# Kernel tuning notes

Measured on AMD Instinct MI355X. Metric: run time of the kernel, lower is better.

The kernel has to match this reference:

```python
import jax, jax.numpy as jnp
import numpy as np

VARIANCE = (0.1, 0.2)   # SSD variance from init_kwargs
TOP_K = 1000            # max detections / NMS candidates per (image, class)


def _pairwise_iou(b):
    # b: [K,4] in point form (x1,y1,x2,y2)
    area = jnp.maximum(b[:, 2] - b[:, 0], 0.0) * jnp.maximum(b[:, 3] - b[:, 1], 0.0)
    lt = jnp.maximum(b[:, None, :2], b[None, :, :2])
    rb = jnp.minimum(b[:, None, 2:], b[None, :, 2:])
    wh = jnp.maximum(rb - lt, 0.0)
    inter = wh[..., 0] * wh[..., 1]
    union = area[:, None] + area[None, :] - inter
    return inter / jnp.maximum(union, 1e-12)


def _nms_pack(points, csboxes, scores, conf_thresh, nms_thresh):
    # points/csboxes: [P,4]; scores: [P]. Returns [TOP_K, 5] = (score, cx, cy, w, h)
    K = TOP_K
    masked = jnp.where(scores >= conf_thresh, scores, -jnp.inf)
    vals, idx = jax.lax.top_k(masked, K)          # sorted descending
    p = points[idx]                                # [K,4] point form
    cs = csboxes[idx]                              # [K,4] center-size form
    valid = vals >= conf_thresh
    iou = _pairwise_iou(p)                         # [K,K]
    ar = jnp.arange(K)

    def body(i, keep):
        # box i (if kept) suppresses all lower-scored boxes with IoU > thresh
        sup = (iou[i] > nms_thresh) & (ar > i) & keep[i]
        return keep & ~sup

    keep = jax.lax.fori_loop(0, K, body, valid)
    rows = jnp.concatenate([vals[:, None], cs], axis=1)        # [K,5]
    pos = jnp.where(keep, jnp.cumsum(keep) - 1, K)             # compact kept rows to front
    out = jnp.zeros((K, 5), rows.dtype).at[pos].set(rows, mode='drop')
    return out


def setup_inputs() -> dict:
    key = jax.random.key(0)
    k1, k2, k3, k4 = jax.random.split(key, 4)
    B, P, C = 8, 120000, 5
    loc_data = jax.random.normal(k1, (B, 4, P), dtype=jnp.float32) * 0.5
    conf_data = jax.random.normal(k2, (B, C, P), dtype=jnp.float32)
    cxcy = jax.random.uniform(k3, (P, 2), dtype=jnp.float32)
    wh = 0.01 + 0.29 * jax.random.uniform(k4, (P, 2), dtype=jnp.float32)
    prior_data = jnp.concatenate([cxcy, wh], axis=1)           # (cx,cy,w,h) in [0,1]
    return {
        'loc_data': loc_data,
        'conf_data': conf_data,
        'prior_data': prior_data,
        'conf_thresh': jnp.float32(0.05),
        'nms_thresh': jnp.float32(0.5),
    }


def reference(loc_data, conf_data, prior_data, conf_thresh, nms_thresh):
    v0, v1 = VARIANCE
    # softmax over class dim, drop background class 0 -> [B, Cfg, P]
    conf = jax.nn.softmax(conf_data, axis=1)[:, 1:]
    loc = jnp.transpose(loc_data, (0, 2, 1))                   # [B,P,4]
    # SSD decode -> center-size boxes
    cxcy = prior_data[None, :, :2] + loc[..., :2] * v0 * prior_data[None, :, 2:]
    wh = prior_data[None, :, 2:] * jnp.exp(loc[..., 2:] * v1)
    cs = jnp.concatenate([cxcy, wh], axis=-1)                  # [B,P,4] center-size
    pts = jnp.concatenate([cxcy - wh / 2, cxcy + wh / 2], axis=-1)  # [B,P,4] point form
    per_class = jax.vmap(_nms_pack, in_axes=(None, None, 0, None, None))
    per_image = jax.vmap(per_class, in_axes=(0, 0, 0, None, None))
    return per_image(pts, cs, conf, conf_thresh, nms_thresh)   # [B, Cfg, TOP_K, 5]
```

## Files before the change

### kernel.cpp

```cpp
#include <hip/hip_runtime.h>
#include <cstdint>
#include <cstddef>

typedef unsigned long long ull;

#define KTOP   1000
#define CAP    4096
#define HBITS  14
#define HB     (1 << HBITS)
#define HSHIFT (32 - HBITS)
#define ROWS   1024
#define WORDS  16
#define HCHUNK 16

__global__ void decode_kernel(const float* __restrict__ loc,
                              const float* __restrict__ conf,
                              const float* __restrict__ prior,
                              float* __restrict__ scores,
                              float* __restrict__ cs,
                              unsigned* __restrict__ histz,
                              int histW,
                              int B, int C, int P) {
#pragma clang fp contract(off)
    int t = blockIdx.x * blockDim.x + threadIdx.x;

    for (int i = t; i < histW; i += gridDim.x * blockDim.x) histz[i] = 0u;

    if (t >= B * P) return;
    int b = t / P;
    int p = t - b * P;

    float x[8];
    float m = -INFINITY;
    for (int c = 0; c < C; ++c) {
        x[c] = conf[((size_t)b * C + c) * P + p];
        m = fmaxf(m, x[c]);
    }
    float sum = 0.f;
    for (int c = 0; c < C; ++c) {
        x[c] = expf(x[c] - m);
        sum += x[c];
    }
    for (int c = 1; c < C; ++c) {
        float v = x[c] / sum;
        int bc = b * (C - 1) + (c - 1);
        scores[(size_t)bc * P + p] = v;
    }

    float l0 = loc[((size_t)b * 4 + 0) * P + p];
    float l1 = loc[((size_t)b * 4 + 1) * P + p];
    float l2 = loc[((size_t)b * 4 + 2) * P + p];
    float l3 = loc[((size_t)b * 4 + 3) * P + p];
    float4 pr4 = *(const float4*)(prior + (size_t)p * 4);

    float cx = pr4.x + (l0 * 0.1f) * pr4.z;
    float cy = pr4.y + (l1 * 0.1f) * pr4.w;
    float w  = pr4.z * expf(l2 * 0.2f);
    float h  = pr4.w * expf(l3 * 0.2f);

    *(float4*)(cs + ((size_t)b * P + p) * 4) = make_float4(cx, cy, w, h);
}

__global__ void __launch_bounds__(256)
hist_kernel(const float* __restrict__ scores,
            const float* __restrict__ cthp,
            unsigned* __restrict__ hist,
            int P) {
    __shared__ unsigned sh[HB / 2];
    int bc  = blockIdx.x;
    int tid = threadIdx.x;
    float cth = *cthp;

    for (int i = tid; i < HB / 2; i += 256) sh[i] = 0u;
    __syncthreads();

    int chunk = (P + HCHUNK - 1) / HCHUNK;
    int lo = blockIdx.y * chunk;
    int hi = lo + chunk; if (hi > P) hi = P;
    const float* s = scores + (size_t)bc * P;
    for (int p = lo + tid; p < hi; p += 256) {
        float v = s[p];
        if (v >= cth) {
            unsigned bin = __float_as_uint(v) >> HSHIFT;
            atomicAdd(&sh[bin >> 1], (bin & 1u) ? 65536u : 1u);
        }
    }
    __syncthreads();

    unsigned* h = hist + (size_t)bc * HB;
    for (int i = tid; i < HB / 2; i += 256) {
        unsigned v = sh[i];
        if (v & 0xFFFFu)  atomicAdd(&h[2 * i],     v & 0xFFFFu);
        if (v >> 16)      atomicAdd(&h[2 * i + 1], v >> 16);
    }
}

__global__ void __launch_bounds__(256)
pivot_kernel(const unsigned* __restrict__ hist, unsigned* __restrict__ pivot) {
    int bc  = blockIdx.x;
    int t   = threadIdx.x;
    const unsigned* h = hist + (size_t)bc * HB;
    __shared__ unsigned T[256];

    const int per = HB / 256;
    int base = t * per;
    unsigned S = 0;
    for (int i = 0; i < per; ++i) S += h[base + i];
    T[t] = S;
    __syncthreads();

    for (int d = 1; d < 256; d <<= 1) {
        unsigned add = (t + d < 256) ? T[t + d] : 0u;
        __syncthreads();
        T[t] += add;
        __syncthreads();
    }

    unsigned Tt = T[t];
    unsigned Tn = (t + 1 < 256) ? T[t + 1] : 0u;
    if (Tt >= (unsigned)KTOP && Tn < (unsigned)KTOP) {
        unsigned cum = Tn;
        for (int i = per - 1; i >= 0; --i) {
            cum += h[base + i];
            if (cum >= (unsigned)KTOP) { pivot[bc] = (unsigned)(base + i); break; }
        }
    }
    if (t == 0 && T[0] < (unsigned)KTOP) pivot[bc] = 0u;
}

__global__ void __launch_bounds__(256)
gather_kernel(const float* __restrict__ scores,
              const unsigned* __restrict__ pivot,
              unsigned* __restrict__ cnt,
              ull* __restrict__ cand,
              const float* __restrict__ cthp, int P) {
    __shared__ unsigned wsum[4];
    __shared__ unsigned s_base;
    int bc = blockIdx.x;
    const float* s = scores + (size_t)bc * P;
    float cth = *cthp;
    unsigned pv = pivot[bc];
    int nchunk = gridDim.y;
    int chunk = (P + nchunk - 1) / nchunk;
    int lo = blockIdx.y * chunk;
    int hi = lo + chunk; if (hi > P) hi = P;
    int tid  = threadIdx.x;
    int lane = tid & 63;
    int wid  = tid >> 6;

    unsigned mycnt = 0;
    for (int p = lo + tid; p < hi; p += 256) {
        float v = s[p];
        unsigned k = __float_as_uint(v);
        if (v >= cth && (k >> HSHIFT) >= pv) ++mycnt;
    }
    unsigned x = mycnt;
    for (int d = 1; d < 64; d <<= 1) {
        unsigned y = (unsigned)__shfl_up((int)x, d);
        if (lane >= d) x += y;
    }
    if (lane == 63) wsum[wid] = x;
    __syncthreads();
    if (tid == 0) {
        unsigned tot = 0;
        for (int w = 0; w < 4; ++w) { unsigned t2 = wsum[w]; wsum[w] = tot; tot += t2; }
        s_base = tot ? atomicAdd(&cnt[bc], tot) : 0u;
    }
    __syncthreads();
    unsigned off = s_base + wsum[wid] + (x - mycnt);

    ull* cb = cand + (size_t)bc * CAP;
    for (int p = lo + tid; p < hi; p += 256) {
        float v = s[p];
        unsigned k = __float_as_uint(v);
        if (v >= cth && (k >> HSHIFT) >= pv) {
            if (off < CAP)
                cb[off] = ((ull)k << 32) | (unsigned)(~(unsigned)p);
            ++off;
        }
    }
}

__global__ void __launch_bounds__(1024)
sort_kernel(const ull* __restrict__ cand,
            const unsigned* __restrict__ cnt,
            const float* __restrict__ cs,
            float* __restrict__ rows,
            float4* __restrict__ pbox,
            float* __restrict__ bar,
            int* __restrict__ nselArr,
            int P, int Cfg) {
#pragma clang fp contract(off)
    int bc  = blockIdx.x;
    int b   = bc / Cfg;
    int tid = threadIdx.x;
    __shared__ ull sbuf[CAP];

    int M = (int)cnt[bc]; if (M > CAP) M = CAP;
    int nsel = M < KTOP ? M : KTOP;
    if (tid == 0) nselArr[bc] = nsel;

    int n = 1024;
    while (n < M) n <<= 1;
    for (int i = tid; i < n; i += 1024)
        sbuf[i] = (i < M) ? cand[(size_t)bc * CAP + i] : 0ull;
    __syncthreads();

    for (unsigned k = 2; k <= (unsigned)n; k <<= 1) {
        for (unsigned j = k >> 1; j > 0; j >>= 1) {
            for (unsigned i = tid; i < (unsigned)n; i += 1024) {
                unsigned ixj = i ^ j;
                if (ixj > i) {
                    bool up = ((i & k) == 0u);
                    ull a = sbuf[i], bb = sbuf[ixj];
                    if ((a > bb) == up) { sbuf[i] = bb; sbuf[ixj] = a; }
                }
            }
            __syncthreads();
        }
    }

    for (int r = tid; r < nsel; r += 1024) {
        ull e = sbuf[n - 1 - r];
        float sc = __uint_as_float((unsigned)(e >> 32));
        int idx = (int)(~(unsigned)e);
        const float* c4 = cs + ((size_t)b * P + idx) * 4;
        float cx = c4[0], cy = c4[1], w = c4[2], h = c4[3];
        float x1 = cx - w / 2.f, y1 = cy - h / 2.f;
        float x2 = cx + w / 2.f, y2 = cy + h / 2.f;
        size_t sb = (size_t)bc * ROWS + r;
        pbox[sb] = make_float4(x1, y1, x2, y2);
        bar[sb]  = fmaxf(x2 - x1, 0.f) * fmaxf(y2 - y1, 0.f);
        float* rr = rows + ((size_t)bc * KTOP + r) * 5;
        rr[0] = sc; rr[1] = cx; rr[2] = cy; rr[3] = w; rr[4] = h;
    }
}

__global__ void __launch_bounds__(1024)
mask_kernel(const float4* __restrict__ pbox,
            const float* __restrict__ bar,
            const int* __restrict__ nselArr,
            const float* __restrict__ nthp,
            ull* __restrict__ mask) {
#pragma clang fp contract(off)
    int bc   = blockIdx.x;
    int tile = blockIdx.y;
    int tid  = threadIdx.x;
    int nsel = nselArr[bc];
    float nth = *nthp;

    __shared__ float4 sbox[ROWS];
    __shared__ float  sar[ROWS];
    size_t sb = (size_t)bc * ROWS;
    sbox[tid] = pbox[sb + tid];
    sar[tid]  = bar[sb + tid];
    __syncthreads();

    int wv   = tid >> 6;
    int lane = tid & 63;
    int i0   = tile * 64 + (wv << 2);

    float4 bi[4]; float ai[4];
    #pragma unroll
    for (int r = 0; r < 4; ++r) { bi[r] = sbox[i0 + r]; ai[r] = sar[i0 + r]; }

    ull rowbits[4] = {0ull, 0ull, 0ull, 0ull};
    for (int w = 0; w < WORDS; ++w) {
        int j = (w << 6) + lane;
        float4 bj = sbox[j];
        float  aj = sar[j];
        #pragma unroll
        for (int r = 0; r < 4; ++r) {
            int i = i0 + r;
            float ww = fmaxf(fminf(bi[r].z, bj.z) - fmaxf(bi[r].x, bj.x), 0.f);
            float hh = fmaxf(fminf(bi[r].w, bj.w) - fmaxf(bi[r].y, bj.y), 0.f);
            float inter = ww * hh;
            float uni = ai[r] + aj - inter;
            float iou = inter / fmaxf(uni, 1e-12f);
            bool ok = (j > i) && (j < nsel) && (iou > nth);
            ull bits = __ballot(ok);
            if (lane == w) rowbits[r] = bits;
        }
    }
    #pragma unroll
    for (int r = 0; r < 4; ++r)
        if (lane < WORDS)
            mask[(((size_t)bc * ROWS + (i0 + r)) << 4) + lane] = rowbits[r];
}

__device__ __forceinline__ void nms_chunk_body(
    int c, int nchunk, int lane, int g, int w,
    const ull* __restrict__ mrow, ull* sm,
    ull (&pr)[16], ull (&st)[16], ull& S)
{
    int cb = (c & 1) << 10;
    int nb = ((c + 1) & 1) << 10;
    if (c + 2 < nchunk) {
        #pragma unroll
        for (int k = 0; k < 16; ++k)
            pr[k] = mrow[(size_t)(c + 2) * 1024 + k * 64 + lane];
    }

    ull cur = __shfl(S, c);
    #pragma unroll
    for (int i = 0; i < 64; ++i) {
        ull di   = sm[cb + (i << 4) + c];
        ull supm = (ull)((long long)(cur << (63 - i)) >> 63);
        cur |= di & ~supm;
    }
    ull kbits = ~cur;

    unsigned sub = (unsigned)((kbits >> (g << 4)) & 0xFFFFull);
    int rbase2 = cb + (g << 8) + w;
    ull part = 0ull;
    #pragma unroll
    for (int i = 0; i < 16; ++i) {
        ull v = sm[rbase2 + (i << 4)];
        part |= v & (ull)(0ll - (long long)((sub >> i) & 1u));
    }
    part |= __shfl_xor(part, 16);
    part |= __shfl_xor(part, 32);
    S |= part;
    if (lane == c) S = cur;

    if (c + 1 < nchunk) {
        #pragma unroll
        for (int k = 0; k < 16; ++k) sm[nb + k * 64 + lane] = st[k];
    }
}

__global__ void __launch_bounds__(256)
reduce_pack_kernel(const ull* __restrict__ mask,
                   const int* __restrict__ nselArr,
                   const float* __restrict__ rows,
                   float* __restrict__ out) {
    int bc  = blockIdx.x;
    int tid = threadIdx.x;
    int nsel = nselArr[bc];
    const ull* mrow = mask + ((size_t)bc * ROWS << 4);

    __shared__ ull sm[2048];
    __shared__ ull kw[WORDS];
    __shared__ unsigned pref[WORDS + 1];

    if (tid < 64) {
        int lane = tid;
        int nchunk = (nsel + 63) >> 6;
        ull S = 0ull;
        int g = lane >> 4;
        int w = lane & 15;

        ull ra[16], rb[16];
        if (nchunk > 0) {
            #pragma unroll
            for (int k = 0; k < 16; ++k) ra[k] = mrow[k * 64 + lane];
            if (nchunk > 1) {
                #pragma unroll
                for (int k = 0; k < 16; ++k) rb[k] = mrow[1024 + k * 64 + lane];
            }
            #pragma unroll
            for (int k = 0; k < 16; ++k) sm[k * 64 + lane] = ra[k];

            #pragma unroll 1
            for (int cc = 0; cc < 8; ++cc) {
                int c0 = cc << 1;
                if (c0 >= nchunk) break;
                nms_chunk_body(c0, nchunk, lane, g, w, mrow, sm, ra, rb, S);
                int c1 = c0 + 1;
                if (c1 >= nchunk) break;
                nms_chunk_body(c1, nchunk, lane, g, w, mrow, sm, rb, ra, S);
            }
        }

        if (lane < WORDS) {
            int base_i = lane << 6;
            ull valid = 0ull;
            int rem = nsel - base_i;
            if (rem > 0) valid = (rem >= 64) ? ~0ull : ((1ull << rem) - 1ull);
            kw[lane] = (~S) & valid;
        }
    }
    __syncthreads();

    if (tid == 0) {
        unsigned c = 0;
        for (int w = 0; w < WORDS; ++w) { pref[w] = c; c += (unsigned)__popcll(kw[w]); }
        pref[WORDS] = c;
    }
    __syncthreads();
    unsigned tot = pref[WORDS];

    const float* rbase = rows + (size_t)bc * KTOP * 5;
    float* obase = out + (size_t)bc * KTOP * 5;
    for (int r = tid; r < KTOP; r += 256) {
        ull wv = kw[r >> 6];
        if ((wv >> (r & 63)) & 1ull) {
            int pos = (int)pref[r >> 6] + __popcll(wv & ((1ull << (r & 63)) - 1ull));
            const float* rr = rbase + r * 5;
            float* oo = obase + pos * 5;
            oo[0] = rr[0]; oo[1] = rr[1]; oo[2] = rr[2]; oo[3] = rr[3]; oo[4] = rr[4];
        }
        if (r >= (int)tot) {
            float* oo = obase + r * 5;
            oo[0] = 0.f; oo[1] = 0.f; oo[2] = 0.f; oo[3] = 0.f; oo[4] = 0.f;
        }
    }
}

extern "C" void kernel_launch(void* const* d_in, const int* in_sizes, int n_in,
                              void* d_out, int out_size, void* d_ws, size_t ws_size,
                              hipStream_t stream) {
    (void)n_in; (void)out_size; (void)ws_size;
    const float* loc   = (const float*)d_in[0];
    const float* conf  = (const float*)d_in[1];
    const float* prior = (const float*)d_in[2];
    const float* cth   = (const float*)d_in[3];
    const float* nth   = (const float*)d_in[4];
    float* out = (float*)d_out;

    int P   = in_sizes[2] / 4;
    int B   = in_sizes[0] / (4 * P);
    int C   = in_sizes[1] / (B * P);
    int Cfg = C - 1;
    int NBC = B * Cfg;

    char* base = (char*)d_ws;
    size_t off = 0;
    auto carve = [&](size_t bytes) { char* p = base + off; off = (off + bytes + 255) & ~(size_t)255; return p; };

    float4*   pbox   = (float4*)  carve((size_t)NBC * ROWS * 16);
    ull*      cand   = (ull*)     carve((size_t)NBC * CAP * 8);
    ull*      mask   = (ull*)     carve((size_t)NBC * ROWS * WORDS * 8);
    float*    scores = (float*)   carve((size_t)NBC * P * 4);
    float*    cs     = (float*)   carve((size_t)B * P * 4 * 4);
    float*    rows   = (float*)   carve((size_t)NBC * KTOP * 5 * 4);
    float*    bar    = (float*)   carve((size_t)NBC * ROWS * 4);
    unsigned* hist   = (unsigned*)carve((size_t)NBC * HB * 4 + (size_t)NBC * 4);
    unsigned* cnt    = hist + (size_t)NBC * HB;
    unsigned* pivot  = (unsigned*)carve((size_t)NBC * 4);
    int*      nselA  = (int*)     carve((size_t)NBC * 4);

    int histW = NBC * HB + NBC;

    int n1 = B * P;
    decode_kernel<<<(n1 + 255) / 256, 256, 0, stream>>>(loc, conf, prior, scores, cs, hist, histW, B, C, P);
    hist_kernel<<<dim3(NBC, HCHUNK), 256, 0, stream>>>(scores, cth, hist, P);
    pivot_kernel<<<NBC, 256, 0, stream>>>(hist, pivot);
    gather_kernel<<<dim3(NBC, 32), 256, 0, stream>>>(scores, pivot, cnt, cand, cth, P);
    sort_kernel<<<NBC, 1024, 0, stream>>>(cand, cnt, cs, rows, pbox, bar, nselA, P, Cfg);
    mask_kernel<<<dim3(NBC, ROWS / 64), 1024, 0, stream>>>(pbox, bar, nselA, nth, mask);
    reduce_pack_kernel<<<NBC, 256, 0, stream>>>(mask, nselA, rows, out);
}
```

Baseline: 221.4 us.

## Pack NMS reduction one wavefront per image-class with transposed padded LDS tile

```diff
diff --git a/kernel.cpp b/kernel.cpp
--- a/kernel.cpp
+++ b/kernel.cpp
@@ -12,6 +12,8 @@
 #define ROWS   1024
 #define WORDS  16
 #define HCHUNK 16
+#define RPW    8
+#define TPW    (WORDS * 66)
 
 __global__ void decode_kernel(const float* __restrict__ loc,
                               const float* __restrict__ conf,
@@ -291,116 +293,113 @@
 __device__ __forceinline__ void nms_chunk_body(
     int c, int nchunk, int lane, int g, int w,
     const ull* __restrict__ mrow, ull* sm,
-    ull (&pr)[16], ull (&st)[16], ull& S)
+    ull (&st)[16], ull& S)
 {
-    int cb = (c & 1) << 10;
-    int nb = ((c + 1) & 1) << 10;
+    #pragma unroll
+    for (int k = 0; k < 16; ++k)
+        sm[w * 66 + (k << 2) + g] = st[k];
+
     if (c + 2 < nchunk) {
         #pragma unroll
         for (int k = 0; k < 16; ++k)
-            pr[k] = mrow[(size_t)(c + 2) * 1024 + k * 64 + lane];
+            st[k] = mrow[(size_t)(c + 2) * 1024 + k * 64 + lane];
     }
 
     ull cur = __shfl(S, c);
+    const ull* diag = sm + c * 66;
     #pragma unroll
     for (int i = 0; i < 64; ++i) {
-        ull di   = sm[cb + (i << 4) + c];
+        ull di   = diag[i];
         ull supm = (ull)((long long)(cur << (63 - i)) >> 63);
         cur |= di & ~supm;
     }
     ull kbits = ~cur;
 
     unsigned sub = (unsigned)((kbits >> (g << 4)) & 0xFFFFull);
-    int rbase2 = cb + (g << 8) + w;
+    const ull* colw = sm + w * 66 + (g << 4);
     ull part = 0ull;
     #pragma unroll
     for (int i = 0; i < 16; ++i) {
-        ull v = sm[rbase2 + (i << 4)];
+        ull v = colw[i];
         part |= v & (ull)(0ll - (long long)((sub >> i) & 1u));
     }
     part |= __shfl_xor(part, 16);
     part |= __shfl_xor(part, 32);
     S |= part;
     if (lane == c) S = cur;
-
-    if (c + 1 < nchunk) {
-        #pragma unroll
-        for (int k = 0; k < 16; ++k) sm[nb + k * 64 + lane] = st[k];
-    }
-}
-
-__global__ void __launch_bounds__(256)
+}
+
+__global__ void __launch_bounds__(RPW * 64)
 reduce_pack_kernel(const ull* __restrict__ mask,
                    const int* __restrict__ nselArr,
                    const float* __restrict__ rows,
-                   float* __restrict__ out) {
-    int bc  = blockIdx.x;
-    int tid = threadIdx.x;
+                   float* __restrict__ out, int NBC) {
+    __shared__ ull smT[RPW * TPW];
+    int wv   = threadIdx.x >> 6;
+    int lane = threadIdx.x & 63;
+    int bc   = blockIdx.x * RPW + wv;
+    if (bc >= NBC) return;
+    ull* sm = smT + wv * TPW;
     int nsel = nselArr[bc];
     const ull* mrow = mask + ((size_t)bc * ROWS << 4);
 
-    __shared__ ull sm[2048];
-    __shared__ ull kw[WORDS];
-    __shared__ unsigned pref[WORDS + 1];
-
-    if (tid < 64) {
-        int lane = tid;
-        int nchunk = (nsel + 63) >> 6;
-        ull S = 0ull;
-        int g = lane >> 4;
-        int w = lane & 15;
-
-        ull ra[16], rb[16];
-        if (nchunk > 0) {
+    int nchunk = (nsel + 63) >> 6;
+    ull S = 0ull;
+    int g = lane >> 4;
+    int w = lane & 15;
+
+    ull ra[16], rb[16];
+    if (nchunk > 0) {
+        #pragma unroll
+        for (int k = 0; k < 16; ++k) ra[k] = mrow[k * 64 + lane];
+        if (nchunk > 1) {
             #pragma unroll
-            for (int k = 0; k < 16; ++k) ra[k] = mrow[k * 64 + lane];
-            if (nchunk > 1) {
-                #pragma unroll
-                for (int k = 0; k < 16; ++k) rb[k] = mrow[1024 + k * 64 + lane];
-            }
-            #pragma unroll
-            for (int k = 0; k < 16; ++k) sm[k * 64 + lane] = ra[k];
-
-            #pragma unroll 1
-            for (int cc = 0; cc < 8; ++cc) {
-                int c0 = cc << 1;
-                if (c0 >= nchunk) break;
-                nms_chunk_body(c0, nchunk, lane, g, w, mrow, sm, ra, rb, S);
-                int c1 = c0 + 1;
-                if (c1 >= nchunk) break;
-                nms_chunk_body(c1, nchunk, lane, g, w, mrow, sm, rb, ra, S);
-            }
-        }
-
-        if (lane < WORDS) {
-            int base_i = lane << 6;
-            ull valid = 0ull;
-            int rem = nsel - base_i;
-            if (rem > 0) valid = (rem >= 64) ? ~0ull : ((1ull << rem) - 1ull);
-            kw[lane] = (~S) & valid;
-        }
-    }
-    __syncthreads();
-
-    if (tid == 0) {
-        unsigned c = 0;
-        for (int w = 0; w < WORDS; ++w) { pref[w] = c; c += (unsigned)__popcll(kw[w]); }
-        pref[WORDS] = c;
-    }
-    __syncthreads();
-    unsigned tot = pref[WORDS];
+            for (int k = 0; k < 16; ++k) rb[k] = mrow[1024 + k * 64 + lane];
+        }
+        #pragma unroll 1
+        for (int cc = 0; cc < 8; ++cc) {
+            int c0 = cc << 1;
+            if (c0 >= nchunk) break;
+            nms_chunk_body(c0, nchunk, lane, g, w, mrow, sm, ra, S);
+            int c1 = c0 + 1;
+            if (c1 >= nchunk) break;
+            nms_chunk_body(c1, nchunk, lane, g, w, mrow, sm, rb, S);
+        }
+    }
+
+    ull K = 0ull;
+    int cnt = 0;
+    if (lane < WORDS) {
+        int base_i = lane << 6;
+        int rem = nsel - base_i;
+        ull valid = 0ull;
+        if (rem > 0) valid = (rem >= 64) ? ~0ull : ((1ull << rem) - 1ull);
+        K = (~S) & valid;
+        cnt = __popcll(K);
+    }
+    int x = cnt;
+    for (int d = 1; d < 64; d <<= 1) {
+        int y = __shfl_up(x, d);
+        if (lane >= d) x += y;
+    }
+    int pref = x - cnt;
+    int tot  = __shfl(x, 63);
 
     const float* rbase = rows + (size_t)bc * KTOP * 5;
     float* obase = out + (size_t)bc * KTOP * 5;
-    for (int r = tid; r < KTOP; r += 256) {
-        ull wv = kw[r >> 6];
-        if ((wv >> (r & 63)) & 1ull) {
-            int pos = (int)pref[r >> 6] + __popcll(wv & ((1ull << (r & 63)) - 1ull));
+    #pragma unroll 1
+    for (int it = 0; it < WORDS; ++it) {
+        int r = (it << 6) + lane;
+        if (r >= KTOP) break;
+        ull kwv   = (ull)__shfl((long long)K, it);
+        int prefw = __shfl(pref, it);
+        if ((kwv >> lane) & 1ull) {
+            int pos = prefw + __popcll(kwv & ((1ull << lane) - 1ull));
             const float* rr = rbase + r * 5;
             float* oo = obase + pos * 5;
             oo[0] = rr[0]; oo[1] = rr[1]; oo[2] = rr[2]; oo[3] = rr[3]; oo[4] = rr[4];
         }
-        if (r >= (int)tot) {
+        if (r >= tot) {
             float* oo = obase + r * 5;
             oo[0] = 0.f; oo[1] = 0.f; oo[2] = 0.f; oo[3] = 0.f; oo[4] = 0.f;
         }
@@ -449,5 +448,5 @@
     gather_kernel<<<dim3(NBC, 32), 256, 0, stream>>>(scores, pivot, cnt, cand, cth, P);
     sort_kernel<<<NBC, 1024, 0, stream>>>(cand, cnt, cs, rows, pbox, bar, nselA, P, Cfg);
     mask_kernel<<<dim3(NBC, ROWS / 64), 1024, 0, stream>>>(pbox, bar, nselA, nth, mask);
-    reduce_pack_kernel<<<NBC, 256, 0, stream>>>(mask, nselA, rows, out);
-}
+    reduce_pack_kernel<<<(NBC + RPW - 1) / RPW, RPW * 64, 0, stream>>>(mask, nselA, rows, out, NBC);
+}
```

Result: no change. 225.6 us (+1.9%).
